# Kernel optimization log

Hardware: AMD Instinct MI355X
Metric: run time of the kernel (lower is better)

Reference implementation:

```python
import jax, jax.numpy as jnp
import numpy as np

B, T, H, D = 4, 4096, 1024, 4  # batch, seq_len, hidden_size, max_depth


def setup_inputs() -> dict:
    key = jax.random.key(0)
    ks = jax.random.split(key, 8)
    s = 1.0 / np.sqrt(H)
    x = jax.random.normal(ks[0], (B, T, H), dtype=jnp.float32)
    state = jax.random.normal(ks[1], (B, D, H), dtype=jnp.float32)
    # time_decay_multi initialized as in the torch module: row d = 0.9**(d+1)
    time_decay_multi = jnp.broadcast_to(
        (0.9 ** jnp.arange(1, D + 1, dtype=jnp.float32))[:, None], (D, H)
    ).astype(jnp.float32)
    Wl = jax.random.uniform(ks[2], (D, H), jnp.float32, -s, s)   # level_selector weight [out=D, in=H]
    bl = jax.random.uniform(ks[3], (D,), jnp.float32, -s, s)
    Wv = jax.random.uniform(ks[4], (H, H), jnp.float32, -s, s)
    Wk = jax.random.uniform(ks[5], (H, H), jnp.float32, -s, s)
    Wr = jax.random.uniform(ks[6], (H, H), jnp.float32, -s, s)
    Wo = jax.random.uniform(ks[7], (H, H), jnp.float32, -s, s)
    return {"x": x, "state": state, "time_decay_multi": time_decay_multi,
            "Wl": Wl, "bl": bl, "Wv": Wv, "Wk": Wk, "Wr": Wr, "Wo": Wo}


def reference(x, state, time_decay_multi, Wl, bl, Wv, Wk, Wr, Wo):
    # Projections (torch Linear: y = x @ W.T)
    v = jnp.einsum('bth,oh->bto', x, Wv)
    k = jnp.einsum('bth,oh->bto', x, Wk)
    r = jax.nn.sigmoid(jnp.einsum('bth,oh->bto', x, Wr))
    level_weights = jax.nn.softmax(jnp.einsum('bth,dh->btd', x, Wl) + bl, axis=-1)  # [B,T,D]

    decay = jnp.exp(-jnp.exp(time_decay_multi))        # [D,H]
    decayed_state0 = state * decay[None]               # [B,D,H] (original state is never updated in the loop)
    kv = k * v                                         # [B,T,H]

    # per-step state for depth d is decayed_state0[b,d] + kv[b,t]; weighted sum over depths:
    weighted = (jnp.einsum('btd,bdh->bth', level_weights, decayed_state0)
                + jnp.sum(level_weights, axis=-1, keepdims=True) * kv)  # [B,T,H]
    o = r * weighted
    output = jnp.einsum('bth,oh->bto', o, Wo)

    # new_state after the loop keeps only the LAST timestep contribution
    new_state = decayed_state0 + kv[:, -1][:, None, :]  # [B,D,H]
    return output, new_state
```

## Files before the change

kernel.cpp:

```cpp
#include <hip/hip_runtime.h>

#define B_ 4
#define T_ 4096
#define H_ 1024
#define D_ 4
#define M_ (B_ * T_)
#define OUT_MAIN (M_ * H_)

#define WS_BUF  0UL
#define WS_WK   33554432UL
#define WS_LGW  41943040UL
#define WS_DEC  42205184UL

typedef __bf16 bf16x8 __attribute__((ext_vector_type(8)));
typedef unsigned short u16x4 __attribute__((ext_vector_type(4)));
typedef float f32x4 __attribute__((ext_vector_type(4)));

__device__ __forceinline__ float b2f(unsigned short u) {
    union { unsigned int i; float f; } c;
    c.i = ((unsigned int)u) << 16;
    return c.f;
}
__device__ __forceinline__ unsigned short f2b(float f) {
    union { float f; unsigned int i; } c;
    c.f = f;
    unsigned int x = c.i;
    unsigned int r = (x + 0x7FFFu + ((x >> 16) & 1u)) >> 16;
    return (unsigned short)r;
}

#define BAR()  asm volatile("s_barrier" ::: "memory")
#define GLLDS(gsrc, ldst)                                                     \
    __builtin_amdgcn_global_load_lds(                                         \
        (const __attribute__((address_space(1))) unsigned int*)(gsrc),        \
        (__attribute__((address_space(3))) unsigned int*)(ldst), 16, 0, 0)

__global__ __launch_bounds__(256) void cvtw_k(
    const float* __restrict__ s0, const float* __restrict__ s1,
    const float* __restrict__ s2, const float* __restrict__ s3,
    unsigned short* __restrict__ d)
{
    const int w = blockIdx.y;
    const float* s = (w == 0) ? s0 : (w == 1) ? s1 : (w == 2) ? s2 : s3;
    const int i = blockIdx.x * 256 + threadIdx.x;
    const f32x4 v = ((const f32x4*)s)[i];
    u16x4 o;
    o[0] = f2b(v[0]); o[1] = f2b(v[1]); o[2] = f2b(v[2]); o[3] = f2b(v[3]);
    ((u16x4*)(d + (size_t)w * (H_ * H_)))[i] = o;
}

__global__ __launch_bounds__(256) void logcvt_k(
    const float* __restrict__ X, const float* __restrict__ Wl,
    const float* __restrict__ bl, float* __restrict__ lgw,
    unsigned short* __restrict__ xb)
{
    const int wid  = threadIdx.x >> 6;
    const int lane = threadIdx.x & 63;
    const int row  = blockIdx.x * 4 + wid;
    const float* xp = X + (size_t)row * H_;
    unsigned short* xo = xb + (size_t)row * H_;

    float acc[D_] = {0.f, 0.f, 0.f, 0.f};
    for (int h = lane * 4; h < H_; h += 256) {
        const f32x4 xv = *(const f32x4*)(xp + h);
        u16x4 xc;
        xc[0] = f2b(xv[0]); xc[1] = f2b(xv[1]);
        xc[2] = f2b(xv[2]); xc[3] = f2b(xv[3]);
        *(u16x4*)(xo + h) = xc;
#pragma unroll
        for (int d = 0; d < D_; ++d) {
            const f32x4 wv = *(const f32x4*)(Wl + d * H_ + h);
            acc[d] += xv[0] * wv[0] + xv[1] * wv[1] + xv[2] * wv[2] + xv[3] * wv[3];
        }
    }
#pragma unroll
    for (int off = 32; off; off >>= 1)
#pragma unroll
        for (int d = 0; d < D_; ++d) acc[d] += __shfl_xor(acc[d], off, 64);

    if (lane == 0) {
        float l[D_];
#pragma unroll
        for (int d = 0; d < D_; ++d) l[d] = acc[d] + bl[d];
        const float mx = fmaxf(fmaxf(l[0], l[1]), fmaxf(l[2], l[3]));
        float e[D_], s = 0.f;
#pragma unroll
        for (int d = 0; d < D_; ++d) { e[d] = __expf(l[d] - mx); s += e[d]; }
        const float inv = 1.0f / s;
        f32x4 o;
#pragma unroll
        for (int d = 0; d < D_; ++d) o[d] = e[d] * inv;
        *(f32x4*)(lgw + (size_t)row * 4) = o;
    }
}

__global__ void decstate_k(const float* __restrict__ state,
                           const float* __restrict__ tdm,
                           float* __restrict__ dec)
{
    const int i = blockIdx.x * blockDim.x + threadIdx.x;
    if (i >= B_ * D_ * H_) return;
    const int dh = i & (D_ * H_ - 1);
    dec[i] = state[i] * __expf(-__expf(tdm[dh]));
}

__global__ __launch_bounds__(256) void newstate_k(
    const float* __restrict__ X, const float* __restrict__ Wk,
    const float* __restrict__ Wv, const float* __restrict__ dec,
    float* __restrict__ out2)
{
    const int wid  = threadIdx.x >> 6;
    const int lane = threadIdx.x & 63;
    const int row  = blockIdx.x * 4 + wid;
    const int b    = row >> 10;
    const int h    = row & (H_ - 1);
    const float* xp = X + ((size_t)(b * T_ + (T_ - 1))) * H_;

    float ak = 0.f, av = 0.f;
    for (int j = lane * 4; j < H_; j += 256) {
        const f32x4 xv = *(const f32x4*)(xp + j);
        const f32x4 wk = *(const f32x4*)(Wk + (size_t)h * H_ + j);
        const f32x4 wv = *(const f32x4*)(Wv + (size_t)h * H_ + j);
        ak += xv[0]*wk[0] + xv[1]*wk[1] + xv[2]*wk[2] + xv[3]*wk[3];
        av += xv[0]*wv[0] + xv[1]*wv[1] + xv[2]*wv[2] + xv[3]*wv[3];
    }
#pragma unroll
    for (int off = 32; off; off >>= 1) {
        ak += __shfl_xor(ak, off, 64);
        av += __shfl_xor(av, off, 64);
    }
    if (lane == 0) {
        const float kv = ak * av;
#pragma unroll
        for (int d = 0; d < D_; ++d)
            out2[(size_t)(b * D_ + d) * H_ + h] = dec[(b * D_ + d) * H_ + h] + kv;
    }
}

__global__ __launch_bounds__(512, 2) void gemm_kvr(
    const unsigned short* __restrict__ A,
    const unsigned short* __restrict__ Wk,
    const unsigned short* __restrict__ Wv,
    const unsigned short* __restrict__ Wr,
    unsigned short* __restrict__ Co,
    const float* __restrict__ lgw,
    const float* __restrict__ dec)
{
    __shared__ __align__(16) unsigned short As [2 * 8192];
    __shared__ __align__(16) unsigned short Bks[2 * 8192];
    __shared__ __align__(16) unsigned short Bvs[2 * 8192];
    __shared__ __align__(16) unsigned short Brs[2 * 8192];

    const int tid  = threadIdx.x;
    const int wid  = tid >> 6;
    const int lane = tid & 63;
    const int l15  = lane & 15;
    const int q    = lane >> 4;
    const int wrow = wid >> 2;
    const int wcol = wid & 3;

    const int lin  = blockIdx.y * 8 + blockIdx.x;
    const int xcd  = lin & 7;
    const int slot = lin >> 3;
    const int brow = (xcd * 16 + (slot >> 3)) * 128;
    const int bcol = (slot & 7) * 128;

    const int g0row = tid >> 3, g0cg = (tid & 7) ^ (g0row & 7);
    const int g1row = 64 + g0row, g1cg = (tid & 7) ^ (g1row & 7);
    const int offA0 = (brow + g0row) * 1024 + g0cg * 8;
    const int offA1 = (brow + g1row) * 1024 + g1cg * 8;
    const int offB0 = (bcol + g0row) * 1024 + g0cg * 8;
    const int offB1 = (bcol + g1row) * 1024 + g1cg * 8;
    const int dst0 = tid * 8;
    const int dst1 = 4096 + tid * 8;

    int gx[2];
#pragma unroll
    for (int ks = 0; ks < 2; ++ks) gx[ks] = ((ks * 4 + q) ^ (l15 & 7)) * 8;
    int aB[4], bB[2];
#pragma unroll
    for (int mi = 0; mi < 4; ++mi) aB[mi] = (wrow * 64 + mi * 16 + l15) * 64;
#pragma unroll
    for (int ni = 0; ni < 2; ++ni) bB[ni] = (wcol * 32 + ni * 16 + l15) * 64;

    f32x4 accK[4][2], accV[4][2], accR[4][2];
#pragma unroll
    for (int i = 0; i < 4; ++i)
#pragma unroll
        for (int j = 0; j < 2; ++j) {
            accK[i][j] = (f32x4){0.f, 0.f, 0.f, 0.f};
            accV[i][j] = (f32x4){0.f, 0.f, 0.f, 0.f};
            accR[i][j] = (f32x4){0.f, 0.f, 0.f, 0.f};
        }

#define SG_A(bo, tau)  do { GLLDS(A  + offA0 + (tau) * 64, As  + (bo) + dst0); \
                            GLLDS(A  + offA1 + (tau) * 64, As  + (bo) + dst1); } while (0)
#define SG_BK(bo, tau) do { GLLDS(Wk + offB0 + (tau) * 64, Bks + (bo) + dst0); \
                            GLLDS(Wk + offB1 + (tau) * 64, Bks + (bo) + dst1); } while (0)
#define SG_BV(bo, tau) do { GLLDS(Wv + offB0 + (tau) * 64, Bvs + (bo) + dst0); \
                            GLLDS(Wv + offB1 + (tau) * 64, Bvs + (bo) + dst1); } while (0)
#define SG_BR(bo, tau) do { GLLDS(Wr + offB0 + (tau) * 64, Brs + (bo) + dst0); \
                            GLLDS(Wr + offB1 + (tau) * 64, Brs + (bo) + dst1); } while (0)
#define RD_AALL(CUR)                                                          \
    _Pragma("unroll") for (int mi = 0; mi < 4; ++mi)                          \
    _Pragma("unroll") for (int ks = 0; ks < 2; ++ks)                          \
        aR[mi][ks] = *(const bf16x8*)&As[(CUR) + aB[mi] + gx[ks]];
#define RD_B(ARR, CUR)                                                        \
    _Pragma("unroll") for (int nj = 0; nj < 2; ++nj)                          \
    _Pragma("unroll") for (int ks = 0; ks < 2; ++ks)                          \
        bR[nj][ks] = *(const bf16x8*)&ARR[(CUR) + bB[nj] + gx[ks]];
#define MFMA16(ACC)                                                           \
    __builtin_amdgcn_s_setprio(1);                                            \
    _Pragma("unroll") for (int mi = 0; mi < 4; ++mi)                          \
    _Pragma("unroll") for (int nj = 0; nj < 2; ++nj)                          \
    _Pragma("unroll") for (int ks = 0; ks < 2; ++ks)                          \
        ACC[mi][nj] = __builtin_amdgcn_mfma_f32_16x16x32_bf16(                \
            aR[mi][ks], bR[nj][ks], ACC[mi][nj], 0, 0, 0);                    \
    __builtin_amdgcn_s_setprio(0);

    SG_A(0, 0); SG_BK(0, 0); SG_BV(0, 0); SG_BR(0, 0);
    asm volatile("s_waitcnt vmcnt(4)" ::: "memory");
    BAR();

#pragma unroll 1
    for (int t = 0; t < 15; ++t) {
        const int cur = (t & 1) << 13;
        const int nxt = cur ^ 8192;
        bf16x8 aR[4][2], bR[2][2];

        RD_AALL(cur); RD_B(Bks, cur);
        SG_A(nxt, t + 1); SG_BK(nxt, t + 1);
        BAR(); MFMA16(accK);
        asm volatile("s_waitcnt vmcnt(6)" ::: "memory");
        BAR();

        RD_B(Bvs, cur);
        SG_BV(nxt, t + 1);
        BAR(); MFMA16(accV);
        asm volatile("s_waitcnt vmcnt(6)" ::: "memory");
        BAR();

        RD_B(Brs, cur);
        SG_BR(nxt, t + 1);
        BAR(); MFMA16(accR);
        asm volatile("s_waitcnt vmcnt(4)" ::: "memory");
        BAR();
    }
    {
        const int cur = 8192;
        bf16x8 aR[4][2], bR[2][2];
        RD_AALL(cur); RD_B(Bks, cur);
        BAR(); MFMA16(accK);
        asm volatile("s_waitcnt vmcnt(2)" ::: "memory");
        BAR();
        RD_B(Bvs, cur);
        BAR(); MFMA16(accV);
        asm volatile("s_waitcnt vmcnt(0)" ::: "memory");
        BAR();
        RD_B(Brs, cur);
        MFMA16(accR);
    }
#undef SG_A
#undef SG_BK
#undef SG_BV
#undef SG_BR
#undef RD_AALL
#undef RD_B
#undef MFMA16

    const int orow0 = brow + wrow * 64;
    const int ocol0 = bcol + wcol * 32;
    const int rbase = q * 4;
    const int b = brow >> 12;
    float dcol[2][4];
#pragma unroll
    for (int ni = 0; ni < 2; ++ni)
#pragma unroll
        for (int d = 0; d < 4; ++d)
            dcol[ni][d] = dec[b * (D_ * H_) + d * H_ + (ocol0 + ni * 16 + l15)];
#pragma unroll
    for (int mi = 0; mi < 4; ++mi)
#pragma unroll
        for (int j = 0; j < 4; ++j) {
            const int r = orow0 + mi * 16 + rbase + j;
            const f32x4 lw = *(const f32x4*)(lgw + (size_t)r * 4);
            const float wsum = lw[0] + lw[1] + lw[2] + lw[3];
#pragma unroll
            for (int ni = 0; ni < 2; ++ni) {
                const size_t idx = (size_t)r * 1024 + (ocol0 + ni * 16 + l15);
                const float kvf = b2f(f2b(accV[mi][ni][j] * b2f(f2b(accK[mi][ni][j]))));
                const float rv  = 1.0f / (1.0f + __expf(-accR[mi][ni][j]));
                const float w   = lw[0] * dcol[ni][0] + lw[1] * dcol[ni][1]
                                + lw[2] * dcol[ni][2] + lw[3] * dcol[ni][3]
                                + wsum * kvf;
                Co[idx] = f2b(rv * w);
            }
        }
}

__global__ __launch_bounds__(512, 2) void gemm_o(
    const unsigned short* __restrict__ A,
    const unsigned short* __restrict__ Wt,
    float* __restrict__ outf)
{
    __shared__ __align__(16) unsigned short As[2 * 256 * 64];
    __shared__ __align__(16) unsigned short Bs[2 * 256 * 64];

    const int tid  = threadIdx.x;
    const int wid  = tid >> 6;
    const int lane = tid & 63;
    const int l15  = lane & 15;
    const int l7   = lane & 7;
    const int wrow = wid >> 2;
    const int wcol = wid & 3;
    const int brow = blockIdx.x * 256;
    const int bcol = blockIdx.y * 256;

    int offA[4], offB[4], dst[4];
#pragma unroll
    for (int i = 0; i < 4; ++i) {
        const int G   = i * 512 + tid;
        const int row = G >> 3;
        const int cg  = (G & 7) ^ (row & 7);
        offA[i] = (brow + row) * 1024 + cg * 8;
        offB[i] = (bcol + row) * 1024 + cg * 8;
        dst[i]  = G * 8;
    }

    int aB[8], bB[4], gx[2];
#pragma unroll
    for (int ks = 0; ks < 2; ++ks) gx[ks] = ((ks * 4 + (lane >> 4)) ^ l7) * 8;
#pragma unroll
    for (int mi = 0; mi < 8; ++mi) aB[mi] = (wrow * 128 + mi * 16 + l15) * 64;
#pragma unroll
    for (int ni = 0; ni < 4; ++ni) bB[ni] = (wcol * 64 + ni * 16 + l15) * 64;

    f32x4 acc[8][4];
#pragma unroll
    for (int i = 0; i < 8; ++i)
#pragma unroll
        for (int j = 0; j < 4; ++j)
            acc[i][j] = (f32x4){0.f, 0.f, 0.f, 0.f};

#pragma unroll
    for (int i = 0; i < 4; ++i) {
        GLLDS(A  + offA[i], As + dst[i]);
        GLLDS(Wt + offB[i], Bs + dst[i]);
    }
    asm volatile("s_waitcnt vmcnt(0)" ::: "memory");
    BAR();

#pragma unroll 1
    for (int t = 0; t < 16; ++t) {
        const int cur = (t & 1) * 16384;
        const int nxt = 16384 - cur;
        const int kk  = (t + 1) * 64;
        const bool st = (t < 15);
        bf16x8 aR[4][2], bR[4][2];

#pragma unroll
        for (int mi = 0; mi < 4; ++mi)
#pragma unroll
            for (int ks = 0; ks < 2; ++ks)
                aR[mi][ks] = *(const bf16x8*)&As[cur + aB[mi] + gx[ks]];
#pragma unroll
        for (int ni = 0; ni < 2; ++ni)
#pragma unroll
            for (int ks = 0; ks < 2; ++ks)
                bR[ni][ks] = *(const bf16x8*)&Bs[cur + bB[ni] + gx[ks]];
        if (st) {
            GLLDS(A  + offA[0] + kk, As + nxt + dst[0]);
            GLLDS(A  + offA[1] + kk, As + nxt + dst[1]);
            GLLDS(Wt + offB[0] + kk, Bs + nxt + dst[0]);
        }
        BAR();
        __builtin_amdgcn_s_setprio(1);
#pragma unroll
        for (int mi = 0; mi < 4; ++mi)
#pragma unroll
            for (int ni = 0; ni < 2; ++ni)
#pragma unroll
                for (int ks = 0; ks < 2; ++ks)
                    acc[mi][ni] = __builtin_amdgcn_mfma_f32_16x16x32_bf16(
                        aR[mi][ks], bR[ni][ks], acc[mi][ni], 0, 0, 0);
        __builtin_amdgcn_s_setprio(0);
        BAR();

#pragma unroll
        for (int ni = 2; ni < 4; ++ni)
#pragma unroll
            for (int ks = 0; ks < 2; ++ks)
                bR[ni][ks] = *(const bf16x8*)&Bs[cur + bB[ni] + gx[ks]];
        if (st) {
            GLLDS(A  + offA[2] + kk, As + nxt + dst[2]);
            GLLDS(A  + offA[3] + kk, As + nxt + dst[3]);
            GLLDS(Wt + offB[1] + kk, Bs + nxt + dst[1]);
        }
        BAR();
        __builtin_amdgcn_s_setprio(1);
#pragma unroll
        for (int mi = 0; mi < 4; ++mi)
#pragma unroll
            for (int ni = 2; ni < 4; ++ni)
#pragma unroll
                for (int ks = 0; ks < 2; ++ks)
                    acc[mi][ni] = __builtin_amdgcn_mfma_f32_16x16x32_bf16(
                        aR[mi][ks], bR[ni][ks], acc[mi][ni], 0, 0, 0);
        __builtin_amdgcn_s_setprio(0);
        BAR();

#pragma unroll
        for (int mi = 0; mi < 4; ++mi)
#pragma unroll
            for (int ks = 0; ks < 2; ++ks)
                aR[mi][ks] = *(const bf16x8*)&As[cur + aB[4 + mi] + gx[ks]];
        if (st) {
            GLLDS(Wt + offB[2] + kk, Bs + nxt + dst[2]);
            GLLDS(Wt + offB[3] + kk, Bs + nxt + dst[3]);
        }
        BAR();
        __builtin_amdgcn_s_setprio(1);
#pragma unroll
        for (int mi = 0; mi < 4; ++mi)
#pragma unroll
            for (int ni = 2; ni < 4; ++ni)
#pragma unroll
                for (int ks = 0; ks < 2; ++ks)
                    acc[4 + mi][ni] = __builtin_amdgcn_mfma_f32_16x16x32_bf16(
                        aR[mi][ks], bR[ni][ks], acc[4 + mi][ni], 0, 0, 0);
        __builtin_amdgcn_s_setprio(0);
        BAR();

        __builtin_amdgcn_s_setprio(1);
#pragma unroll
        for (int mi = 0; mi < 4; ++mi)
#pragma unroll
            for (int ni = 0; ni < 2; ++ni)
#pragma unroll
                for (int ks = 0; ks < 2; ++ks)
                    acc[4 + mi][ni] = __builtin_amdgcn_mfma_f32_16x16x32_bf16(
                        aR[mi][ks], bR[ni][ks], acc[4 + mi][ni], 0, 0, 0);
        __builtin_amdgcn_s_setprio(0);
        asm volatile("s_waitcnt vmcnt(0)" ::: "memory");
        BAR();
    }

    const int orow0 = brow + wrow * 128;
    const int ocol0 = bcol + wcol * 64;
    const int rbase = (lane >> 4) * 4;
#pragma unroll
    for (int mi = 0; mi < 8; ++mi)
#pragma unroll
        for (int j = 0; j < 4; ++j) {
            const size_t r = (size_t)(orow0 + mi * 16 + rbase + j);
#pragma unroll
            for (int ni = 0; ni < 4; ++ni)
                outf[r * 1024 + (ocol0 + ni * 16 + l15)] = acc[mi][ni][j];
        }
}

extern "C" void kernel_launch(void* const* d_in, const int* in_sizes, int n_in,
                              void* d_out, int out_size, void* d_ws, size_t ws_size,
                              hipStream_t stream)
{
    const float* x   = (const float*)d_in[0];
    const float* st  = (const float*)d_in[1];
    const float* tdm = (const float*)d_in[2];
    const float* Wl  = (const float*)d_in[3];
    const float* bl  = (const float*)d_in[4];
    const float* Wv  = (const float*)d_in[5];
    const float* Wk  = (const float*)d_in[6];
    const float* Wr  = (const float*)d_in[7];
    const float* Wo  = (const float*)d_in[8];
    float* out = (float*)d_out;

    char* ws = (char*)d_ws;
    unsigned short* buf  = (unsigned short*)(ws + WS_BUF);
    unsigned short* wk_b = (unsigned short*)(ws + WS_WK);
    unsigned short* wv_b = wk_b + 1 * (H_ * H_);
    unsigned short* wr_b = wk_b + 2 * (H_ * H_);
    unsigned short* wo_b = wk_b + 3 * (H_ * H_);
    float* lgw = (float*)(ws + WS_LGW);
    float* dec = (float*)(ws + WS_DEC);

    unsigned short* xb = (unsigned short*)out;

    decstate_k<<<(B_ * D_ * H_ + 255) / 256, 256, 0, stream>>>(st, tdm, dec);
    logcvt_k<<<M_ / 4, 256, 0, stream>>>(x, Wl, bl, lgw, xb);
    newstate_k<<<(B_ * H_) / 4, 256, 0, stream>>>(x, Wk, Wv, dec, out + OUT_MAIN);
    cvtw_k<<<dim3(1024, 4), 256, 0, stream>>>(Wk, Wv, Wr, Wo, wk_b);

    gemm_kvr<<<dim3(H_ / 128, M_ / 128), 512, 0, stream>>>(
        xb, wk_b, wv_b, wr_b, buf, lgw, dec);

    gemm_o<<<dim3(M_ / 256, H_ / 256), 512, 0, stream>>>(buf, wo_b, out);
}
```

Measured before the change: 175.4 us.

## Software-pipeline LDS reads ahead of MFMAs in fused KVR GEMM main loop

Restructures the fused K/V/R GEMM main loop so the next tile's A and B fragments are read from shared memory into a second register set while the current tile's MFMAs run. Global-to-LDS prefetch is issued two tiles ahead, and the loop is unrolled by two with ping-pong register arrays. The aim is to hide LDS read latency and cut barrier stalls between the three MFMA phases. The cost is higher register pressure from the doubled A fragments, which could lower occupancy, and a more fragile wait-count schedule. The launch grid is written as literal constants equal to the old expression.

```diff
diff --git a/kernel.cpp b/kernel.cpp
--- a/kernel.cpp
+++ b/kernel.cpp
@@ -193,6 +193,8 @@
             accR[i][j] = (f32x4){0.f, 0.f, 0.f, 0.f};
         }
 
+    bf16x8 aR0[4][2], aR1[4][2], bk[2][2], bv[2][2], br[2][2];
+
 #define SG_A(bo, tau)  do { GLLDS(A  + offA0 + (tau) * 64, As  + (bo) + dst0); \
                             GLLDS(A  + offA1 + (tau) * 64, As  + (bo) + dst1); } while (0)
 #define SG_BK(bo, tau) do { GLLDS(Wk + offB0 + (tau) * 64, Bks + (bo) + dst0); \
@@ -201,72 +203,76 @@
                             GLLDS(Wv + offB1 + (tau) * 64, Bvs + (bo) + dst1); } while (0)
 #define SG_BR(bo, tau) do { GLLDS(Wr + offB0 + (tau) * 64, Brs + (bo) + dst0); \
                             GLLDS(Wr + offB1 + (tau) * 64, Brs + (bo) + dst1); } while (0)
-#define RD_AALL(CUR)                                                          \
+#define RD_AALL(DST, CUR)                                                     \
     _Pragma("unroll") for (int mi = 0; mi < 4; ++mi)                          \
     _Pragma("unroll") for (int ks = 0; ks < 2; ++ks)                          \
-        aR[mi][ks] = *(const bf16x8*)&As[(CUR) + aB[mi] + gx[ks]];
-#define RD_B(ARR, CUR)                                                        \
+        DST[mi][ks] = *(const bf16x8*)&As[(CUR) + aB[mi] + gx[ks]];
+#define RDB2(DST, ARR, CUR)                                                   \
     _Pragma("unroll") for (int nj = 0; nj < 2; ++nj)                          \
     _Pragma("unroll") for (int ks = 0; ks < 2; ++ks)                          \
-        bR[nj][ks] = *(const bf16x8*)&ARR[(CUR) + bB[nj] + gx[ks]];
-#define MFMA16(ACC)                                                           \
+        DST[nj][ks] = *(const bf16x8*)&ARR[(CUR) + bB[nj] + gx[ks]];
+#define MFMA16A(ACC, AARR, BARR)                                              \
     __builtin_amdgcn_s_setprio(1);                                            \
     _Pragma("unroll") for (int mi = 0; mi < 4; ++mi)                          \
     _Pragma("unroll") for (int nj = 0; nj < 2; ++nj)                          \
     _Pragma("unroll") for (int ks = 0; ks < 2; ++ks)                          \
         ACC[mi][nj] = __builtin_amdgcn_mfma_f32_16x16x32_bf16(                \
-            aR[mi][ks], bR[nj][ks], ACC[mi][nj], 0, 0, 0);                    \
+            AARR[mi][ks], BARR[nj][ks], ACC[mi][nj], 0, 0, 0);                \
     __builtin_amdgcn_s_setprio(0);
 
+#define TILE(T, CUR, NXT, ARC, ARN)                                           \
+                \
+    RDB2(bv, Bvs, CUR);                                                       \
+    SG_BV(NXT, (T) + 1); SG_BR(NXT, (T) + 1);                                 \
+    BAR(); MFMA16A(accK, ARC, bk); BAR();                                     \
+        \
+    RDB2(br, Brs, CUR);                                                       \
+    SG_A(CUR, (T) + 2); SG_BK(CUR, (T) + 2);                                  \
+    BAR(); MFMA16A(accV, ARC, bv);                                            \
+    asm volatile("s_waitcnt vmcnt(8)" ::: "memory");    \
+    BAR();                                                                    \
+                                      \
+    RD_AALL(ARN, NXT); RDB2(bk, Bks, NXT);                                    \
+    BAR(); MFMA16A(accR, ARC, br);                                            \
+    asm volatile("s_waitcnt vmcnt(4)" ::: "memory");   \
+    BAR();
+
     SG_A(0, 0); SG_BK(0, 0); SG_BV(0, 0); SG_BR(0, 0);
+    SG_A(8192, 1); SG_BK(8192, 1);
     asm volatile("s_waitcnt vmcnt(4)" ::: "memory");
     BAR();
+    RD_AALL(aR0, 0); RDB2(bk, Bks, 0);
 
 #pragma unroll 1
-    for (int t = 0; t < 15; ++t) {
-        const int cur = (t & 1) << 13;
-        const int nxt = cur ^ 8192;
-        bf16x8 aR[4][2], bR[2][2];
-
-        RD_AALL(cur); RD_B(Bks, cur);
-        SG_A(nxt, t + 1); SG_BK(nxt, t + 1);
-        BAR(); MFMA16(accK);
-        asm volatile("s_waitcnt vmcnt(6)" ::: "memory");
-        BAR();
-
-        RD_B(Bvs, cur);
-        SG_BV(nxt, t + 1);
-        BAR(); MFMA16(accV);
-        asm volatile("s_waitcnt vmcnt(6)" ::: "memory");
-        BAR();
-
-        RD_B(Brs, cur);
-        SG_BR(nxt, t + 1);
-        BAR(); MFMA16(accR);
-        asm volatile("s_waitcnt vmcnt(4)" ::: "memory");
-        BAR();
-    }
-    {
-        const int cur = 8192;
-        bf16x8 aR[4][2], bR[2][2];
-        RD_AALL(cur); RD_B(Bks, cur);
-        BAR(); MFMA16(accK);
-        asm volatile("s_waitcnt vmcnt(2)" ::: "memory");
-        BAR();
-        RD_B(Bvs, cur);
-        BAR(); MFMA16(accV);
-        asm volatile("s_waitcnt vmcnt(0)" ::: "memory");
-        BAR();
-        RD_B(Brs, cur);
-        MFMA16(accR);
-    }
+    for (int t = 0; t < 14; t += 2) {
+        TILE(t,     0,    8192, aR0, aR1)
+        TILE(t + 1, 8192, 0,    aR1, aR0)
+    }
+    RDB2(bv, Bvs, 0);
+    SG_BV(8192, 15); SG_BR(8192, 15);
+    BAR(); MFMA16A(accK, aR0, bk); BAR();
+    RDB2(br, Brs, 0);
+    BAR(); MFMA16A(accV, aR0, bv);
+    asm volatile("s_waitcnt vmcnt(4)" ::: "memory");
+    BAR();
+    RD_AALL(aR1, 8192); RDB2(bk, Bks, 8192);
+    BAR(); MFMA16A(accR, aR0, br);
+    asm volatile("s_waitcnt vmcnt(0)" ::: "memory");
+    BAR();
+    RDB2(bv, Bvs, 8192);
+    MFMA16A(accK, aR1, bk);
+    RDB2(br, Brs, 8192);
+    MFMA16A(accV, aR1, bv);
+    MFMA16A(accR, aR1, br);
+
 #undef SG_A
 #undef SG_BK
 #undef SG_BV
 #undef SG_BR
 #undef RD_AALL
-#undef RD_B
-#undef MFMA16
+#undef RDB2
+#undef MFMA16A
+#undef TILE
 
     const int orow0 = brow + wrow * 64;
     const int ocol0 = bcol + wcol * 32;
@@ -490,7 +496,7 @@
     newstate_k<<<(B_ * H_) / 4, 256, 0, stream>>>(x, Wk, Wv, dec, out + OUT_MAIN);
     cvtw_k<<<dim3(1024, 4), 256, 0, stream>>>(Wk, Wv, Wr, Wo, wk_b);
 
-    gemm_kvr<<<dim3(H_ / 128, M_ / 128), 512, 0, stream>>>(
+    gemm_kvr<<<dim3(8, 128), 512, 0, stream>>>(
         xb, wk_b, wv_b, wr_b, buf, lgw, dec);
 
     gemm_o<<<dim3(M_ / 256, H_ / 256), 512, 0, stream>>>(buf, wo_b, out);
```

New measurement: 189.8 us. +8.2%, slower.
